# Performance work log

Measured on AMD Instinct MI355X. Metric: run time of the kernel, lower is better.

The kernel has to match this reference:

```python
import jax, jax.numpy as jnp
import numpy as np

B, EMB, ARRAY = 4096, 512, 2
KW = KH = KC = 8
OC = 16                      # output_channel per branch
RED = OC * 2                 # SE hidden width
NUM_REL = 500
FC_IN = 3 * OC * KH * KW * KC  # 24576, flattened concat of 3 branches


def _make_chequer_perm():
    # Deterministic replication of MSLE.get_chequer_perm (perm=1).
    rng = np.random.RandomState(0)
    ent_perm = rng.permutation(EMB * (ARRAY - 1))
    rel_perm = rng.permutation(EMB)
    idxs, ei, ri = [], 0, 0
    for i in range(KC):
        for j in range(KH):
            for k in range(KW):
                for m in range(ARRAY):
                    if (i + j) % ARRAY == m:
                        idxs.append(int(rel_perm[ri]) + EMB * (ARRAY - 1)); ri += 1
                    else:
                        idxs.append(int(ent_perm[ei])); ei += 1
    return jnp.asarray(np.asarray(idxs, dtype=np.int32))


def setup_inputs() -> dict:
    key = jax.random.key(0)
    ks = jax.random.split(key, 12)
    n = lambda k, shape, s=0.05: jax.random.normal(k, shape, jnp.float32) * s
    f1_dim = ARRAY * OC * 1 * 1 * ARRAY        # (1,1,2) kernels
    f3_dim = ARRAY * OC * 1 * ARRAY * ARRAY    # (1,2,2) kernels
    f5_dim = ARRAY * OC * ARRAY * ARRAY * ARRAY  # (2,2,2) kernels
    z = lambda shape: jnp.zeros(shape, jnp.float32)
    o = lambda shape: jnp.ones(shape, jnp.float32)
    return {
        "concat_input": jax.random.normal(ks[0], (B, EMB * ARRAY), jnp.float32),
        "rel": jax.random.randint(ks[1], (B,), 0, NUM_REL),
        "chequer_perm": _make_chequer_perm(),
        "f1_table": n(ks[2], (NUM_REL, f1_dim)),
        "f3_table": n(ks[3], (NUM_REL, f3_dim)),
        "f5_table": n(ks[4], (NUM_REL, f5_dim)),
        "bn0_g": o((ARRAY,)), "bn0_b": z((ARRAY,)),
        "bn1_g": o((OC,)), "bn1_b": z((OC,)),
        "bn2_g": o((OC,)), "bn2_b": z((OC,)),
        "bn3_g": o((OC,)), "bn3_b": z((OC,)),
        "att_Wsq": n(ks[5], (OC, RED)), "att_bsq": z((RED,)),
        "att_W1": n(ks[6], (RED, OC)), "att_b1": z((OC,)),
        "att_W2": n(ks[7], (RED, OC)), "att_b2": z((OC,)),
        "att_W3": n(ks[8], (RED, OC)), "att_b3": z((OC,)),
        "fc_W": n(ks[9], (FC_IN, EMB), 0.01), "fc_b": z((EMB,)),
    }


def _bn(x, g, b, eps=1e-5):
    # BatchNorm3d, training-mode batch statistics over (N, D, H, W).
    m = x.mean(axis=(0, 2, 3, 4), keepdims=True)
    v = x.var(axis=(0, 2, 3, 4), keepdims=True)
    sh = (1, -1, 1, 1, 1)
    return (x - m) * jax.lax.rsqrt(v + eps) * g.reshape(sh) + b.reshape(sh)


def _per_sample_conv(x, w):
    # x: (B, Cin, D, H, W); w: (B, Cout, Cin, kd, kh, kw). 'same' padding,
    # even kernels pad the extra element at the high end (torch padding='same').
    conv1 = lambda xb, wb: jax.lax.conv_general_dilated(
        xb[None], wb, (1, 1, 1), 'SAME',
        dimension_numbers=('NCDHW', 'OIDHW', 'NCDHW'))[0]
    return jax.vmap(conv1)(x, w)


def reference(concat_input, rel, chequer_perm, f1_table, f3_table, f5_table,
              bn0_g, bn0_b, bn1_g, bn1_b, bn2_g, bn2_b, bn3_g, bn3_b,
              att_Wsq, att_bsq, att_W1, att_b1, att_W2, att_b2, att_W3, att_b3,
              fc_W, fc_b):
    b = concat_input.shape[0]
    # Chequered interleave of entity / relation embedding dims.
    x = concat_input[:, chequer_perm].reshape(b, ARRAY, KW, KH, KC)
    x = _bn(x, bn0_g, bn0_b)  # dropout = identity (eval)
    # Per-sample dynamic filters from relation embeddings.
    f1 = f1_table[rel].reshape(b, OC, ARRAY, 1, 1, ARRAY)
    f3 = f3_table[rel].reshape(b, OC, ARRAY, 1, ARRAY, ARRAY)
    f5 = f5_table[rel].reshape(b, OC, ARRAY, ARRAY, ARRAY, ARRAY)
    x1 = _bn(_per_sample_conv(x, f1), bn1_g, bn1_b)
    x3 = _bn(_per_sample_conv(x, f3), bn2_g, bn2_b)
    x5 = _bn(_per_sample_conv(x, f5), bn3_g, bn3_b)
    xs = x1 + x3 + x5
    # SE-style 3D attention: global pool -> shared squeeze -> 3 sigmoid gates.
    pooled = xs.mean(axis=(2, 3, 4))                       # (B, OC)
    zq = jax.nn.relu(pooled @ att_Wsq + att_bsq)           # (B, RED)
    gate = lambda W, bb: jax.nn.sigmoid(zq @ W + bb)[:, :, None, None, None]
    x1 = x1 * gate(att_W1, att_b1)
    x3 = x3 * gate(att_W2, att_b2)
    x5 = x5 * gate(att_W3, att_b3)
    out = jax.nn.relu(jnp.concatenate([x1, x3, x5], axis=1))
    out = out.reshape(b, -1)                               # (B, FC_IN)
    return out @ fc_W + fc_b                               # (B, EMB)
```

## Files before the change

### kernel.cpp

```cpp
#include <hip/hip_runtime.h>
#include <hip/hip_bf16.h>
#include <stdint.h>

typedef short s16x8 __attribute__((ext_vector_type(8)));
typedef short s16x4 __attribute__((ext_vector_type(4)));
typedef float f32x4 __attribute__((ext_vector_type(4)));

#define NB 4096
#define KTOT 24576
#define NOUT 512
#define NCH 48

__device__ __forceinline__ short f2bf(float f){
  union { float f; uint32_t u; } x; x.f = f;
  uint32_t r = (x.u + 0x7FFFu + ((x.u >> 16) & 1u)) >> 16;
  return (short)r;
}
__device__ __forceinline__ float bf2f(short s){
  union { uint32_t u; float f; } x; x.u = ((uint32_t)(uint16_t)s) << 16;
  return x.f;
}
__device__ __forceinline__ short f2bf_fast(float x){
  union { __hip_bfloat16 h; short s; } c; c.h = __float2bfloat16(x); return c.s;
}

#define GLOAD16(g, l) __builtin_amdgcn_global_load_lds( \
  (const __attribute__((address_space(1))) void*)(g), \
  (__attribute__((address_space(3))) void*)(l), 16, 0, 0)

__global__ __launch_bounds__(256) void k_colmap(const int* __restrict__ perm,
                                                int* __restrict__ chmap,
                                                float* __restrict__ statf){
  int q = blockIdx.x * 256 + threadIdx.x;
  if (q < 1024) chmap[perm[q]] = q >> 9;
  if (blockIdx.x == 0 && threadIdx.x < 4) statf[threadIdx.x] = 0.f;
}

__global__ __launch_bounds__(256) void k_bn0(const float* __restrict__ concat,
                                             const int* __restrict__ chmap,
                                             float* __restrict__ statf){
  int t = threadIdx.x;
  float s0=0,q0=0,s1=0,q1=0;
  for (int idx = blockIdx.x*256 + t; idx < NB*1024; idx += gridDim.x*256){
    float v = concat[idx];
    int ch = chmap[idx & 1023];
    if (ch){ s1 += v; q1 += v*v; } else { s0 += v; q0 += v*v; }
  }
  #pragma unroll
  for (int m=1;m<64;m<<=1){
    s0 += __shfl_xor(s0,m); q0 += __shfl_xor(q0,m);
    s1 += __shfl_xor(s1,m); q1 += __shfl_xor(q1,m);
  }
  __shared__ float lb[4][4];
  int wid = t>>6, lane = t&63;
  if (lane==0){ lb[wid][0]=s0; lb[wid][1]=q0; lb[wid][2]=s1; lb[wid][3]=q1; }
  __syncthreads();
  if (t==0){
    float a0=0,a1=0,a2=0,a3=0;
    #pragma unroll
    for (int w=0;w<4;w++){ a0+=lb[w][0]; a1+=lb[w][1]; a2+=lb[w][2]; a3+=lb[w][3]; }
    atomicAdd(&statf[0],a0); atomicAdd(&statf[1],a1);
    atomicAdd(&statf[2],a2); atomicAdd(&statf[3],a3);
  }
}

__global__ __launch_bounds__(256) void k_wcast(const float* __restrict__ fcW,
                                               short* __restrict__ wTs){
  __shared__ float tile[64][65];
  int bid = blockIdx.x;
  int kb = (bid % 384) * 64;
  int nb = (bid / 384) * 64;
  int t = threadIdx.x;
  #pragma unroll
  for (int i=0;i<16;i++){
    int r = i*4 + (t>>6), c = t & 63;
    tile[r][c] = fcW[(size_t)(kb + r)*NOUT + nb + c];
  }
  __syncthreads();
  #pragma unroll
  for (int i=0;i<16;i++){
    int n = i*4 + (t>>6), k = t & 63;
    int nr = nb + n;
    int ks = (((k>>3) ^ (nr&7))<<3) | (k&7);
    wTs[(size_t)nr*KTOT + kb + ks] = f2bf(tile[k][n]);
  }
}

__global__ __launch_bounds__(256) void k_conv(
    const float* __restrict__ concat, const int* __restrict__ perm,
    const int* __restrict__ rel,
    const float* __restrict__ f1t, const float* __restrict__ f3t,
    const float* __restrict__ f5t,
    const float* __restrict__ statf,
    const float* __restrict__ bn0g, const float* __restrict__ bn0b,
    short* __restrict__ raw, float* __restrict__ psum, float* __restrict__ psq)
{
  const int b = blockIdx.x;
  const int t = threadIdx.x;
  __shared__ float xn[2*9*9*9];
  __shared__ float filt[448];
  for (int i=t;i<1458;i+=256) xn[i]=0.f;
  int r = rel[b];
  for (int i=t;i<448;i+=256){
    float v;
    if (i < 64)       v = f1t[r*64 + i];
    else if (i < 192) v = f3t[r*128 + (i-64)];
    else              v = f5t[r*256 + (i-192)];
    filt[i]=v;
  }
  __syncthreads();
  const float n0inv = 1.f/(4096.f*512.f);
  float m0 = statf[0]*n0inv, e0 = statf[1]*n0inv;
  float m1 = statf[2]*n0inv, e1 = statf[3]*n0inv;
  float sc0 = bn0g[0]*rsqrtf(e0-m0*m0+1e-5f), sh0 = bn0b[0]-m0*sc0;
  float sc1 = bn0g[1]*rsqrtf(e1-m1*m1+1e-5f), sh1 = bn0b[1]-m1*sc1;
  for (int q=t;q<1024;q+=256){
    int col = perm[q];
    float v = concat[(size_t)b*1024 + col];
    int ch = q>>9, s = q & 511;
    int d = s>>6, h=(s>>3)&7, w=s&7;
    xn[ch*729 + d*81 + h*9 + w] = ch ? v*sc1+sh1 : v*sc0+sh0;
  }
  __syncthreads();

  const int wid = t>>6, lane = t&63;
  const int d = lane>>3, h = lane&7;
  float r00[9], r01[9], r10[9], r11[9], r20[9], r21[9], r30[9], r31[9];
  #pragma unroll
  for (int w9=0;w9<9;w9++){
    int base0 = d*81 + h*9 + w9;
    int base1 = d*81 + (h+1)*9 + w9;
    int base2 = (d+1)*81 + h*9 + w9;
    int base3 = (d+1)*81 + (h+1)*9 + w9;
    r00[w9]=xn[base0];      r01[w9]=xn[729+base0];
    r10[w9]=xn[base1];      r11[w9]=xn[729+base1];
    r20[w9]=xn[base2];      r21[w9]=xn[729+base2];
    r30[w9]=xn[base3];      r31[w9]=xn[729+base3];
  }
  const size_t rawbase = (size_t)b*KTOT;

  auto finish = [&](int c, const float* v){
    float s=0,q=0;
    #pragma unroll
    for (int p=0;p<8;p++){ s += v[p]; q += v[p]*v[p]; }
    #pragma unroll
    for (int m=1;m<64;m<<=1){ s += __shfl_xor(s,m); q += __shfl_xor(q,m); }
    if (lane==0){ psum[c*NB+b]=s; psq[c*NB+b]=q; }
    s16x8 pk;
    #pragma unroll
    for (int p=0;p<8;p++) pk[p] = f2bf_fast(v[p]);
    *reinterpret_cast<s16x8*>(raw + rawbase + (size_t)c*512 + lane*8) = pk;
  };

  #pragma unroll
  for (int i=0;i<4;i++){
    int oc = wid + 4*i;
    float c0=filt[oc*4+0], c1=filt[oc*4+1], c2=filt[oc*4+2], c3=filt[oc*4+3];
    float v[8];
    #pragma unroll
    for (int p=0;p<8;p++)
      v[p] = c0*r00[p]+c1*r00[p+1]+c2*r01[p]+c3*r01[p+1];
    finish(oc, v);
  }
  #pragma unroll
  for (int i=0;i<4;i++){
    int oc = wid + 4*i;
    const float* cf = &filt[64 + oc*8];
    float v[8];
    #pragma unroll
    for (int p=0;p<8;p++)
      v[p] = cf[0]*r00[p]+cf[1]*r00[p+1]+cf[2]*r10[p]+cf[3]*r10[p+1]
           + cf[4]*r01[p]+cf[5]*r01[p+1]+cf[6]*r11[p]+cf[7]*r11[p+1];
    finish(16+oc, v);
  }
  #pragma unroll
  for (int i=0;i<4;i++){
    int oc = wid + 4*i;
    const float* cf = &filt[192 + oc*16];
    float v[8];
    #pragma unroll
    for (int p=0;p<8;p++)
      v[p] = cf[0]*r00[p] +cf[1]*r00[p+1] +cf[2]*r10[p] +cf[3]*r10[p+1]
           + cf[4]*r20[p] +cf[5]*r20[p+1] +cf[6]*r30[p] +cf[7]*r30[p+1]
           + cf[8]*r01[p] +cf[9]*r01[p+1] +cf[10]*r11[p]+cf[11]*r11[p+1]
           + cf[12]*r21[p]+cf[13]*r21[p+1]+cf[14]*r31[p]+cf[15]*r31[p+1];
    finish(32+oc, v);
  }
}

__global__ __launch_bounds__(256) void k_bnstats(
    const float* __restrict__ psum, const float* __restrict__ psq,
    const float* __restrict__ bn1g, const float* __restrict__ bn1b,
    const float* __restrict__ bn2g, const float* __restrict__ bn2b,
    const float* __restrict__ bn3g, const float* __restrict__ bn3b,
    float* __restrict__ statf)
{
  int c = blockIdx.x, t = threadIdx.x;
  float s=0,q=0;
  for (int b=t;b<NB;b+=256){ s += psum[c*NB+b]; q += psq[c*NB+b]; }
  #pragma unroll
  for (int m=1;m<64;m<<=1){ s += __shfl_xor(s,m); q += __shfl_xor(q,m); }
  __shared__ float lb[4][2];
  int wid = t>>6, lane = t&63;
  if (lane==0){ lb[wid][0]=s; lb[wid][1]=q; }
  __syncthreads();
  if (t==0){
    s = lb[0][0]+lb[1][0]+lb[2][0]+lb[3][0];
    q = lb[0][1]+lb[1][1]+lb[2][1]+lb[3][1];
    float n = 4096.f*512.f;
    float mean = s/n, var = q/n - mean*mean;
    const float* g  = c<16 ? bn1g : (c<32 ? bn2g : bn3g);
    const float* bb = c<16 ? bn1b : (c<32 ? bn2b : bn3b);
    int oc = c & 15;
    float sc = g[oc]*rsqrtf(var + 1e-5f);
    statf[16+c] = sc;
    statf[64+c] = bb[oc] - mean*sc;
  }
}

__global__ __launch_bounds__(64) void k_se(
    const float* __restrict__ psum, const float* __restrict__ statf,
    const float* __restrict__ Wsq, const float* __restrict__ bsq,
    const float* __restrict__ W1, const float* __restrict__ b1,
    const float* __restrict__ W2, const float* __restrict__ b2,
    const float* __restrict__ W3, const float* __restrict__ b3,
    float* __restrict__ gates)
{
  int b = blockIdx.x, lane = threadIdx.x;
  __shared__ float pooled[16];
  __shared__ float zq[32];
  if (lane < 16){
    float p = 0.f;
    #pragma unroll
    for (int br=0;br<3;br++){
      int c = br*16 + lane;
      p += psum[c*NB+b]*(1.f/512.f)*statf[16+c] + statf[64+c];
    }
    pooled[lane] = p;
  }
  __syncthreads();
  if (lane < 32){
    float z = bsq[lane];
    #pragma unroll
    for (int oc=0;oc<16;oc++) z += pooled[oc]*Wsq[oc*32+lane];
    zq[lane] = fmaxf(z, 0.f);
  }
  __syncthreads();
  if (lane < 48){
    int br = lane>>4, oc = lane&15;
    const float* W  = br==0 ? W1 : (br==1 ? W2 : W3);
    const float* bb = br==0 ? b1 : (br==1 ? b2 : b3);
    float g = bb[oc];
    #pragma unroll
    for (int r2=0;r2<32;r2++) g += zq[r2]*W[r2*16+oc];
    gates[lane*NB + b] = 1.f/(1.f + expf(-g));
  }
}

__global__ __launch_bounds__(512, 2) void k_gemm(
    const short* __restrict__ raw, const short* __restrict__ wTs,
    const float* __restrict__ scale, const float* __restrict__ shift,
    const float* __restrict__ gates, short* __restrict__ partials)
{
  const int t = threadIdx.x;
  const int bid = blockIdx.x;
  const int sk = bid >> 5, rem = bid & 31;
  const int nblk = rem >> 4, mblk = rem & 15;
  const int b0 = mblk*256, n0 = nblk*256;
  const int kb0 = sk*3072;

  __shared__ short Al[2][256*64];
  __shared__ short Wl[2][256*64];
  __shared__ float gsc[6*256];
  __shared__ float gsh[6*256];

  const int wid = t>>6, lane = t&63;
  const int wm = wid>>2, wn = wid&3;
  const int fr = lane&15, fkq = lane>>4;
  const int sbase = fkq ^ (fr&7);

  for (int i=t; i<1536; i+=512){
    int c = i>>8, r2 = i&255;
    int ch = sk*6 + c;
    float g = gates[(size_t)ch*NB + b0 + r2];
    gsc[i] = scale[ch]*g;
    gsh[i] = shift[ch]*g;
  }
  __syncthreads();

  const int ar = t>>1, ah = t&1;
  const short* aptr = raw + (size_t)(b0+ar)*KTOT + kb0 + ah*32;
  const int arow7 = ar & 7;
  const short* wbase = wTs + (size_t)(n0 + wid*32)*KTOT + kb0;
  const int wl_row = lane>>3, wl_g = lane&7;

  f32x4 acc[8][4];
  #pragma unroll
  for (int m=0;m<8;m++)
    #pragma unroll
    for (int n=0;n<4;n++){ f32x4 z = {0.f,0.f,0.f,0.f}; acc[m][n]=z; }

  s16x8 aR[4];

  {
    s16x8 aR0[4];
    #pragma unroll
    for (int i=0;i<4;i++) aR0[i] = *reinterpret_cast<const s16x8*>(aptr + i*8);
    asm volatile("" ::: "memory");
    #pragma unroll
    for (int i=0;i<4;i++)
      GLOAD16(wbase + (size_t)(i*8 + wl_row)*KTOT + wl_g*8, &Wl[0][(wid*32 + i*8)*64]);
    asm volatile("" ::: "memory");
    #pragma unroll
    for (int i=0;i<4;i++) aR[i] = *reinterpret_cast<const s16x8*>(aptr + 64 + i*8);
    asm volatile("" ::: "memory");
    #pragma unroll
    for (int i=0;i<4;i++)
      GLOAD16(wbase + (size_t)(i*8 + wl_row)*KTOT + 64 + wl_g*8, &Wl[1][(wid*32 + i*8)*64]);
    asm volatile("s_waitcnt vmcnt(12)" ::: "memory");
    const float scg = gsc[ar], shg = gsh[ar];
    #pragma unroll
    for (int i=0;i<4;i++){
      s16x8 av;
      #pragma unroll
      for (int j=0;j<8;j++)
        av[j] = f2bf_fast(fmaxf(bf2f(aR0[i][j])*scg + shg, 0.f));
      int slot = (ah*4 + i) ^ arow7;
      *reinterpret_cast<s16x8*>(&Al[0][ar*64 + slot*8]) = av;
    }
    asm volatile("s_waitcnt lgkmcnt(0)" ::: "memory");
    __builtin_amdgcn_s_barrier();
  }

  int cur = 0;
  for (int it=0; it<47; ++it){
    asm volatile("s_waitcnt vmcnt(8)" ::: "memory");
    const short* Ac = &Al[cur][0];
    const short* Wc = &Wl[cur][0];
    #pragma unroll
    for (int ks=0; ks<2; ks++){
      const int so = ((sbase ^ (ks<<2))<<3);
      s16x8 af[8], bf[4];
      #pragma unroll
      for (int m=0;m<8;m++)
        af[m] = *reinterpret_cast<const s16x8*>(Ac + (wm*128 + m*16 + fr)*64 + so);
      #pragma unroll
      for (int n=0;n<4;n++)
        bf[n] = *reinterpret_cast<const s16x8*>(Wc + (wn*64 + n*16 + fr)*64 + so);
      __builtin_amdgcn_s_setprio(1);
      #pragma unroll
      for (int m=0;m<8;m++)
        #pragma unroll
        for (int n=0;n<4;n++)
          acc[m][n] = __builtin_amdgcn_mfma_f32_16x16x32_bf16(af[m], bf[n], acc[m][n], 0,0,0);
      __builtin_amdgcn_s_setprio(0);
    }
    asm volatile("s_waitcnt vmcnt(4)" ::: "memory");
    {
      const int c = (it+1)>>3;
      const float scg = gsc[c*256 + ar], shg = gsh[c*256 + ar];
      short* An = &Al[cur^1][0];
      #pragma unroll
      for (int i=0;i<4;i++){
        s16x8 av;
        #pragma unroll
        for (int j=0;j<8;j++)
          av[j] = f2bf_fast(fmaxf(bf2f(aR[i][j])*scg + shg, 0.f));
        int slot = (ah*4 + i) ^ arow7;
        *reinterpret_cast<s16x8*>(An + ar*64 + slot*8) = av;
      }
    }
    asm volatile("s_waitcnt lgkmcnt(0)" ::: "memory");
    __builtin_amdgcn_s_barrier();
    if (it < 46){
      const int ko = (it+2)*64;
      #pragma unroll
      for (int i=0;i<4;i++) aR[i] = *reinterpret_cast<const s16x8*>(aptr + ko + i*8);
      asm volatile("" ::: "memory");
      #pragma unroll
      for (int i=0;i<4;i++)
        GLOAD16(wbase + (size_t)(i*8 + wl_row)*KTOT + ko + wl_g*8, &Wl[cur][(wid*32 + i*8)*64]);
      asm volatile("" ::: "memory");
    }
    cur ^= 1;
  }
  asm volatile("s_waitcnt vmcnt(0)" ::: "memory");
  {
    const short* Ac = &Al[cur][0];
    const short* Wc = &Wl[cur][0];
    #pragma unroll
    for (int ks=0; ks<2; ks++){
      const int so = ((sbase ^ (ks<<2))<<3);
      s16x8 af[8], bf[4];
      #pragma unroll
      for (int m=0;m<8;m++)
        af[m] = *reinterpret_cast<const s16x8*>(Ac + (wm*128 + m*16 + fr)*64 + so);
      #pragma unroll
      for (int n=0;n<4;n++)
        bf[n] = *reinterpret_cast<const s16x8*>(Wc + (wn*64 + n*16 + fr)*64 + so);
      __builtin_amdgcn_s_setprio(1);
      #pragma unroll
      for (int m=0;m<8;m++)
        #pragma unroll
        for (int n=0;n<4;n++)
          acc[m][n] = __builtin_amdgcn_mfma_f32_16x16x32_bf16(af[m], bf[n], acc[m][n], 0,0,0);
      __builtin_amdgcn_s_setprio(0);
    }
  }

  short* pb = partials + (size_t)sk*NB*NOUT;
  #pragma unroll
  for (int m=0;m<8;m++){
    #pragma unroll
    for (int j=0;j<4;j++){
      int row = b0 + wm*128 + m*16 + fkq*4 + j;
      short* prow = pb + (size_t)row*NOUT + n0 + wn*64 + fr;
      #pragma unroll
      for (int n=0;n<4;n++) prow[n*16] = f2bf_fast(acc[m][n][j]);
    }
  }
}

__global__ __launch_bounds__(256) void k_red(const short* __restrict__ partials,
                                             const float* __restrict__ fcb,
                                             float* __restrict__ out){
  int i = blockIdx.x*256 + threadIdx.x;
  int base = i*4;
  f32x4 v = *reinterpret_cast<const f32x4*>(fcb + (base & 511));
  #pragma unroll
  for (int sk=0;sk<8;sk++){
    s16x4 p = *reinterpret_cast<const s16x4*>(partials + (size_t)sk*2097152 + base);
    v[0] += bf2f(p[0]); v[1] += bf2f(p[1]);
    v[2] += bf2f(p[2]); v[3] += bf2f(p[3]);
  }
  *reinterpret_cast<f32x4*>(out + base) = v;
}

extern "C" void kernel_launch(void* const* d_in, const int* in_sizes, int n_in,
                              void* d_out, int out_size, void* d_ws, size_t ws_size,
                              hipStream_t stream) {
  const float* concat = (const float*)d_in[0];
  const int*   rel    = (const int*)  d_in[1];
  const int*   perm   = (const int*)  d_in[2];
  const float* f1t = (const float*)d_in[3];
  const float* f3t = (const float*)d_in[4];
  const float* f5t = (const float*)d_in[5];
  const float* bn0g=(const float*)d_in[6],  *bn0b=(const float*)d_in[7];
  const float* bn1g=(const float*)d_in[8],  *bn1b=(const float*)d_in[9];
  const float* bn2g=(const float*)d_in[10], *bn2b=(const float*)d_in[11];
  const float* bn3g=(const float*)d_in[12], *bn3b=(const float*)d_in[13];
  const float* Wsq=(const float*)d_in[14],  *bsq=(const float*)d_in[15];
  const float* W1=(const float*)d_in[16],   *b1=(const float*)d_in[17];
  const float* W2=(const float*)d_in[18],   *b2=(const float*)d_in[19];
  const float* W3=(const float*)d_in[20],   *b3=(const float*)d_in[21];
  const float* fcW=(const float*)d_in[22],  *fcb=(const float*)d_in[23];
  float* out = (float*)d_out;
  char* ws = (char*)d_ws;

  const size_t off_raw  = 0;
  const size_t off_wT   = 201326592;
  const size_t off_part = 226492416;
  const size_t off_psum = 260046848;
  const size_t off_psq  = 260833280;
  const size_t off_gate = 261619712;
  const size_t off_stat = 262406144;
  const size_t off_chm  = 262406656;
  const size_t need     = off_chm + 4096;
  if (ws_size < need) return;

  short* raw      = (short*)(ws + off_raw);
  short* wTs      = (short*)(ws + off_wT);
  short* partials = (short*)(ws + off_part);
  float* psum     = (float*)(ws + off_psum);
  float* psq      = (float*)(ws + off_psq);
  float* gates    = (float*)(ws + off_gate);
  float* statf    = (float*)(ws + off_stat);
  int*   chmap    = (int*)  (ws + off_chm);

  k_colmap<<<4, 256, 0, stream>>>(perm, chmap, statf);
  k_bn0   <<<2048, 256, 0, stream>>>(concat, chmap, statf);
  k_wcast <<<3072, 256, 0, stream>>>(fcW, wTs);
  k_conv  <<<4096, 256, 0, stream>>>(concat, perm, rel, f1t, f3t, f5t,
                                     statf, bn0g, bn0b, raw, psum, psq);
  k_bnstats<<<48, 256, 0, stream>>>(psum, psq, bn1g, bn1b, bn2g, bn2b,
                                    bn3g, bn3b, statf);
  k_se    <<<4096, 64, 0, stream>>>(psum, statf, Wsq, bsq, W1, b1, W2, b2,
                                    W3, b3, gates);
  k_gemm  <<<256, 512, 0, stream>>>(raw, wTs, statf+16, statf+64, gates, partials);
  k_red   <<<2048, 256, 0, stream>>>(partials, fcb, out);
}
```

Measured before the change: 358.1 us.

## Restructure GEMM main loop into four-quadrant ping-pong schedule with register gates

The GEMM main loop is split into four quadrant MFMA phases, each bracketed by barriers. Global weight loads, LDS fragment reads and the activation transform are interleaved between those phases, which lets the waves overlap memory traffic with matrix work. The per-row gate scale and shift values now live in registers instead of shared memory, removing the initial block sync and the LDS table. The cost is many more barriers per iteration, a deeper prefetch of A tiles (three ahead) and hand-tuned vmcnt counts that could be fragile or cause stalls. Tile loads near the end of the loop may also reach past the split-K slice.

```diff
diff --git a/kernel.cpp b/kernel.cpp
--- a/kernel.cpp
+++ b/kernel.cpp
@@ -271,28 +271,28 @@
 
   __shared__ short Al[2][256*64];
   __shared__ short Wl[2][256*64];
-  __shared__ float gsc[6*256];
-  __shared__ float gsh[6*256];
 
   const int wid = t>>6, lane = t&63;
   const int wm = wid>>2, wn = wid&3;
   const int fr = lane&15, fkq = lane>>4;
-  const int sbase = fkq ^ (fr&7);
-
-  for (int i=t; i<1536; i+=512){
-    int c = i>>8, r2 = i&255;
+  const int fr7 = fr&7;
+
+  const int ar = t>>1, ah = t&1;
+  const int arow7 = ar & 7;
+  const short* aptr = raw + (size_t)(b0+ar)*KTOT + kb0 + ah*32;
+
+  float gsc[6], gsh[6];
+  #pragma unroll
+  for (int c=0;c<6;c++){
     int ch = sk*6 + c;
-    float g = gates[(size_t)ch*NB + b0 + r2];
-    gsc[i] = scale[ch]*g;
-    gsh[i] = shift[ch]*g;
-  }
-  __syncthreads();
-
-  const int ar = t>>1, ah = t&1;
-  const short* aptr = raw + (size_t)(b0+ar)*KTOT + kb0 + ah*32;
-  const int arow7 = ar & 7;
-  const short* wbase = wTs + (size_t)(n0 + wid*32)*KTOT + kb0;
-  const int wl_row = lane>>3, wl_g = lane&7;
+    float g = gates[(size_t)ch*NB + b0 + ar];
+    gsc[c] = scale[ch]*g;
+    gsh[c] = shift[ch]*g;
+  }
+  asm volatile("s_waitcnt vmcnt(0)" ::: "memory");
+
+  const int wrowbase = (wid>>1)*64 + (wid&1)*16;
+  const int wsrow = lane>>3, wsg = lane&7;
 
   f32x4 acc[8][4];
   #pragma unroll
@@ -300,112 +300,113 @@
     #pragma unroll
     for (int n=0;n<4;n++){ f32x4 z = {0.f,0.f,0.f,0.f}; acc[m][n]=z; }
 
-  s16x8 aR[4];
+  s16x8 af[4][2], bfr[2][2][2], aR[2][4];
+
+  #define AISSUE(tile, dst) { \
+    const short* p_ = aptr + (tile)*64; \
+    _Pragma("unroll") \
+    for (int i_=0;i_<4;i_++) (dst)[i_] = *reinterpret_cast<const s16x8*>(p_ + i_*8); }
+
+  #define WISSUE(tile, h, Wbuf) { \
+    _Pragma("unroll") \
+    for (int i_=0;i_<2;i_++){ \
+      int rr_ = wrowbase + (h)*32 + i_*8; \
+      GLOAD16(wTs + (size_t)(n0+rr_+wsrow)*KTOT + kb0 + (tile)*64 + wsg*8, \
+              &(Wbuf)[rr_*64]); } }
+
+  #define XFORM(src, c, An) { \
+    float sc_ = gsc[c], sh_ = gsh[c]; \
+    _Pragma("unroll") \
+    for (int i_=0;i_<4;i_++){ \
+      s16x8 av_; \
+      _Pragma("unroll") \
+      for (int j_=0;j_<8;j_++) av_[j_] = f2bf_fast(fmaxf(bf2f((src)[i_][j_])*sc_+sh_, 0.f)); \
+      int slot_ = (ah*4+i_) ^ arow7; \
+      *reinterpret_cast<s16x8*>(&(An)[ar*64 + slot_*8]) = av_; } }
+
+  #define RD_A(Ab, mh) { \
+    _Pragma("unroll") \
+    for (int m_=0;m_<4;m_++){ \
+      int row_ = wm*128 + (mh)*64 + m_*16 + fr; \
+      _Pragma("unroll") \
+      for (int k_=0;k_<2;k_++){ \
+        int slot_ = ((k_<<2)|fkq) ^ fr7; \
+        af[m_][k_] = *reinterpret_cast<const s16x8*>(&(Ab)[row_*64 + slot_*8]); } } }
+
+  #define RD_B(Wb, nh) { \
+    _Pragma("unroll") \
+    for (int n_=0;n_<2;n_++){ \
+      int row_ = wn*64 + (nh)*32 + n_*16 + fr; \
+      _Pragma("unroll") \
+      for (int k_=0;k_<2;k_++){ \
+        int slot_ = ((k_<<2)|fkq) ^ fr7; \
+        bfr[nh][n_][k_] = *reinterpret_cast<const s16x8*>(&(Wb)[row_*64 + slot_*8]); } } }
+
+  #define MMQ(mh, nh) { \
+    __builtin_amdgcn_s_setprio(1); \
+    _Pragma("unroll") \
+    for (int k_=0;k_<2;k_++) \
+      _Pragma("unroll") \
+      for (int m_=0;m_<4;m_++) \
+        _Pragma("unroll") \
+        for (int n_=0;n_<2;n_++) \
+          acc[(mh)*4+m_][(nh)*2+n_] = __builtin_amdgcn_mfma_f32_16x16x32_bf16( \
+            af[m_][k_], bfr[nh][n_][k_], acc[(mh)*4+m_][(nh)*2+n_], 0,0,0); \
+    __builtin_amdgcn_s_setprio(0); }
+
+  #define BARRIER __builtin_amdgcn_s_barrier()
+  #define LGKM0 asm volatile("s_waitcnt lgkmcnt(0)" ::: "memory")
+  #define FENCE asm volatile("" ::: "memory")
 
   {
     s16x8 aR0[4];
-    #pragma unroll
-    for (int i=0;i<4;i++) aR0[i] = *reinterpret_cast<const s16x8*>(aptr + i*8);
-    asm volatile("" ::: "memory");
-    #pragma unroll
-    for (int i=0;i<4;i++)
-      GLOAD16(wbase + (size_t)(i*8 + wl_row)*KTOT + wl_g*8, &Wl[0][(wid*32 + i*8)*64]);
-    asm volatile("" ::: "memory");
-    #pragma unroll
-    for (int i=0;i<4;i++) aR[i] = *reinterpret_cast<const s16x8*>(aptr + 64 + i*8);
-    asm volatile("" ::: "memory");
-    #pragma unroll
-    for (int i=0;i<4;i++)
-      GLOAD16(wbase + (size_t)(i*8 + wl_row)*KTOT + 64 + wl_g*8, &Wl[1][(wid*32 + i*8)*64]);
+    AISSUE(0, aR0); FENCE;
+    WISSUE(0, 0, Wl[0]); WISSUE(0, 1, Wl[0]); FENCE;
+    asm volatile("s_waitcnt vmcnt(4)" ::: "memory");
+    XFORM(aR0, 0, Al[0]); FENCE;
+    AISSUE(1, aR[1]); FENCE;
+    WISSUE(1, 0, Wl[1]); WISSUE(1, 1, Wl[1]); FENCE;
+    AISSUE(2, aR[0]); FENCE;
+    LGKM0;
+    BARRIER;
+  }
+
+  int cur = 0;
+  for (int it=0; it<48; ++it){
+    short* Ac = Al[cur];
+    short* Wc = Wl[cur];
+    short* An = Al[cur^1];
+    int c1 = (it+1)>>3; c1 = c1>5 ? 5 : c1;
+    const int parity = (it+1)&1;
+
     asm volatile("s_waitcnt vmcnt(12)" ::: "memory");
-    const float scg = gsc[ar], shg = gsh[ar];
-    #pragma unroll
-    for (int i=0;i<4;i++){
-      s16x8 av;
-      #pragma unroll
-      for (int j=0;j<8;j++)
-        av[j] = f2bf_fast(fmaxf(bf2f(aR0[i][j])*scg + shg, 0.f));
-      int slot = (ah*4 + i) ^ arow7;
-      *reinterpret_cast<s16x8*>(&Al[0][ar*64 + slot*8]) = av;
-    }
-    asm volatile("s_waitcnt lgkmcnt(0)" ::: "memory");
-    __builtin_amdgcn_s_barrier();
-  }
-
-  int cur = 0;
-  for (int it=0; it<47; ++it){
-    asm volatile("s_waitcnt vmcnt(8)" ::: "memory");
-    const short* Ac = &Al[cur][0];
-    const short* Wc = &Wl[cur][0];
-    #pragma unroll
-    for (int ks=0; ks<2; ks++){
-      const int so = ((sbase ^ (ks<<2))<<3);
-      s16x8 af[8], bf[4];
-      #pragma unroll
-      for (int m=0;m<8;m++)
-        af[m] = *reinterpret_cast<const s16x8*>(Ac + (wm*128 + m*16 + fr)*64 + so);
-      #pragma unroll
-      for (int n=0;n<4;n++)
-        bf[n] = *reinterpret_cast<const s16x8*>(Wc + (wn*64 + n*16 + fr)*64 + so);
-      __builtin_amdgcn_s_setprio(1);
-      #pragma unroll
-      for (int m=0;m<8;m++)
-        #pragma unroll
-        for (int n=0;n<4;n++)
-          acc[m][n] = __builtin_amdgcn_mfma_f32_16x16x32_bf16(af[m], bf[n], acc[m][n], 0,0,0);
-      __builtin_amdgcn_s_setprio(0);
-    }
-    asm volatile("s_waitcnt vmcnt(4)" ::: "memory");
-    {
-      const int c = (it+1)>>3;
-      const float scg = gsc[c*256 + ar], shg = gsh[c*256 + ar];
-      short* An = &Al[cur^1][0];
-      #pragma unroll
-      for (int i=0;i<4;i++){
-        s16x8 av;
-        #pragma unroll
-        for (int j=0;j<8;j++)
-          av[j] = f2bf_fast(fmaxf(bf2f(aR[i][j])*scg + shg, 0.f));
-        int slot = (ah*4 + i) ^ arow7;
-        *reinterpret_cast<s16x8*>(An + ar*64 + slot*8) = av;
-      }
-    }
-    asm volatile("s_waitcnt lgkmcnt(0)" ::: "memory");
-    __builtin_amdgcn_s_barrier();
-    if (it < 46){
-      const int ko = (it+2)*64;
-      #pragma unroll
-      for (int i=0;i<4;i++) aR[i] = *reinterpret_cast<const s16x8*>(aptr + ko + i*8);
-      asm volatile("" ::: "memory");
-      #pragma unroll
-      for (int i=0;i<4;i++)
-        GLOAD16(wbase + (size_t)(i*8 + wl_row)*KTOT + ko + wl_g*8, &Wl[cur][(wid*32 + i*8)*64]);
-      asm volatile("" ::: "memory");
-    }
+    RD_A(Ac, 0);
+    RD_B(Wc, 0);
+    BARRIER; LGKM0;
+    MMQ(0, 0);
+    BARRIER;
+
+    WISSUE(it+2, 0, Wc); FENCE;
+    RD_B(Wc, 1);
+    asm volatile("s_waitcnt vmcnt(10)" ::: "memory");
+    if (parity) { XFORM(aR[1], c1, An); } else { XFORM(aR[0], c1, An); }
+    BARRIER; LGKM0;
+    MMQ(0, 1);
+    BARRIER;
+
+    WISSUE(it+2, 1, Wc); FENCE;
+    RD_A(Ac, 1);
+    BARRIER; LGKM0;
+    MMQ(1, 0);
+    BARRIER;
+
+    if (parity) { AISSUE(it+3, aR[1]); } else { AISSUE(it+3, aR[0]); }
+    FENCE;
+    BARRIER; LGKM0;
+    MMQ(1, 1);
+    BARRIER;
+
     cur ^= 1;
-  }
-  asm volatile("s_waitcnt vmcnt(0)" ::: "memory");
-  {
-    const short* Ac = &Al[cur][0];
-    const short* Wc = &Wl[cur][0];
-    #pragma unroll
-    for (int ks=0; ks<2; ks++){
-      const int so = ((sbase ^ (ks<<2))<<3);
-      s16x8 af[8], bf[4];
-      #pragma unroll
-      for (int m=0;m<8;m++)
-        af[m] = *reinterpret_cast<const s16x8*>(Ac + (wm*128 + m*16 + fr)*64 + so);
-      #pragma unroll
-      for (int n=0;n<4;n++)
-        bf[n] = *reinterpret_cast<const s16x8*>(Wc + (wn*64 + n*16 + fr)*64 + so);
-      __builtin_amdgcn_s_setprio(1);
-      #pragma unroll
-      for (int m=0;m<8;m++)
-        #pragma unroll
-        for (int n=0;n<4;n++)
-          acc[m][n] = __builtin_amdgcn_mfma_f32_16x16x32_bf16(af[m], bf[n], acc[m][n], 0,0,0);
-      __builtin_amdgcn_s_setprio(0);
-    }
   }
 
   short* pb = partials + (size_t)sk*NB*NOUT;
@@ -419,6 +420,15 @@
       for (int n=0;n<4;n++) prow[n*16] = f2bf_fast(acc[m][n][j]);
     }
   }
+  #undef AISSUE
+  #undef WISSUE
+  #undef XFORM
+  #undef RD_A
+  #undef RD_B
+  #undef MMQ
+  #undef BARRIER
+  #undef LGKM0
+  #undef FENCE
 }
 
 __global__ __launch_bounds__(256) void k_red(const short* __restrict__ partials,
```

Result: slower. 594.3 us (+66.0%).
